# Optimization experiments

Measured on AMD Instinct MI355X. Metric: run time of the kernel, lower is better.

Reference implementation:

```python
import jax, jax.numpy as jnp
import numpy as np

B, C, N = 64, 512, 512  # batch, channels (=in_dim), last dim (=in_dim)
OUT = 512
GROUPS = 32
EPS = 1e-5


def setup_inputs() -> dict:
    key = jax.random.key(0)
    ks = jax.random.split(key, 7)
    s = 1.0 / np.sqrt(C)
    return {
        "x": jax.random.normal(ks[0], (B, C, N), dtype=jnp.float32),
        "q_w": jax.random.normal(ks[1], (OUT, C), dtype=jnp.float32) * s,
        "q_b": jax.random.normal(ks[2], (OUT,), dtype=jnp.float32) * s,
        "k_w": jax.random.normal(ks[3], (OUT, C), dtype=jnp.float32) * s,
        "k_b": jax.random.normal(ks[4], (OUT,), dtype=jnp.float32) * s,
        "v_w": jax.random.normal(ks[5], (OUT, C), dtype=jnp.float32) * s,
        "v_b": jax.random.normal(ks[6], (OUT,), dtype=jnp.float32) * s,
        "gn_w": jnp.ones((C,), dtype=jnp.float32),
        "gn_b": jnp.zeros((C,), dtype=jnp.float32),
    }


def group_norm(x, w, b):
    # x: (B, C, N); 32 groups over channel dim, affine per-channel.
    Bb, Cc, Nn = x.shape
    xg = x.reshape(Bb, GROUPS, -1)
    mean = jnp.mean(xg, axis=-1, keepdims=True)
    var = jnp.var(xg, axis=-1, keepdims=True)
    xn = ((xg - mean) * jax.lax.rsqrt(var + EPS)).reshape(Bb, Cc, Nn)
    return xn * w[None, :, None] + b[None, :, None]


def reference(x, q_w, q_b, k_w, k_b, v_w, v_b, gn_w, gn_b):
    xn = group_norm(x, gn_w, gn_b)  # (B, C, N)
    # nn.Linear applies to the last dim (N == in_dim)
    q = jnp.einsum("bcn,dn->bcd", xn, q_w) + q_b  # (B, C, OUT)
    k = jnp.einsum("bcn,dn->bcd", xn, k_w) + k_b
    v = jnp.einsum("bcn,dn->bcd", xn, v_w) + v_b
    scale = 1.0 / jnp.sqrt(jnp.float32(OUT))
    scores = jnp.einsum("bqd,bkd->bqk", q, k) * scale  # (B, C, C)
    attn = jax.nn.softmax(scores, axis=-1)
    return jnp.einsum("bqk,bkd->bqd", attn, v)  # (B, C, OUT)
```

## Files before the change

kernel.cpp:

```cpp
#include <hip/hip_runtime.h>
#include <cstdint>

#define EPSV 1e-5f
#define SM_SCALE 0.044194173824159216f

typedef unsigned short u16;
typedef __attribute__((ext_vector_type(8))) short short8;
typedef __attribute__((ext_vector_type(4))) float f32x4;
typedef __attribute__((ext_vector_type(4))) unsigned short us4;

__device__ __forceinline__ u16 f2bf(float f) {
  union { float f; uint32_t u; } v; v.f = f;
  return (u16)((v.u + 0x7FFFu + ((v.u >> 16) & 1u)) >> 16);
}

__device__ __forceinline__ void gload_lds16(const void* g, void* l) {
  __builtin_amdgcn_global_load_lds((const __attribute__((address_space(1))) void*)g,
                                   (__attribute__((address_space(3))) void*)l, 16, 0, 0);
}

__device__ __forceinline__ f32x4 mfma16(short8 a, short8 b, f32x4 c) {
  return __builtin_amdgcn_mfma_f32_16x16x32_bf16(a, b, c, 0, 0, 0);
}

#define WAIT_ENTER(N, is_tail)                                      \
  if (is_tail) { asm volatile("s_waitcnt vmcnt(0)" ::: "memory"); } \
  else         { asm volatile("s_waitcnt vmcnt(" #N ")" ::: "memory"); } \
  __builtin_amdgcn_s_barrier();                                     \
  asm volatile("" ::: "memory");

#define WAIT_EXIT()                                                 \
  asm volatile("s_waitcnt lgkmcnt(0)" ::: "memory");                \
  __builtin_amdgcn_s_barrier();                                     \
  asm volatile("" ::: "memory");

__global__ __launch_bounds__(256) void gn_fused_k(const float* __restrict__ x,
                                                  const float* __restrict__ gw,
                                                  const float* __restrict__ gb,
                                                  u16* __restrict__ xn) {
  __shared__ float xs[8192];
  __shared__ float ls[4], lss[4];
  const int bg = blockIdx.x;
  const int g = bg & 31;
  const float* p = x + (size_t)bg * 8192;
  float s = 0.f, ss = 0.f;
#pragma unroll
  for (int i = 0; i < 8; ++i) {
    const int idx = i * 1024 + threadIdx.x * 4;
    float4 v = *reinterpret_cast<const float4*>(p + idx);
    *reinterpret_cast<float4*>(xs + idx) = v;
    s += v.x + v.y + v.z + v.w;
    ss += v.x * v.x + v.y * v.y + v.z * v.z + v.w * v.w;
  }
  for (int off = 32; off; off >>= 1) { s += __shfl_xor(s, off); ss += __shfl_xor(ss, off); }
  const int w = threadIdx.x >> 6;
  if ((threadIdx.x & 63) == 0) { ls[w] = s; lss[w] = ss; }
  __syncthreads();
  s = ls[0] + ls[1] + ls[2] + ls[3];
  ss = lss[0] + lss[1] + lss[2] + lss[3];
  const float inv_n = 1.0f / 8192.f;
  const float mean = s * inv_n;
  const float rstd = rsqrtf(ss * inv_n - mean * mean + EPSV);
#pragma unroll
  for (int j = 0; j < 4; ++j) {
    const int idx = j * 2048 + threadIdx.x * 8;
    const int c = g * 16 + (idx >> 9);
    const float sc = gw[c] * rstd;
    const float sh = gb[c] - mean * sc;
    u16 o[8];
#pragma unroll
    for (int e = 0; e < 8; ++e) o[e] = f2bf(xs[idx + e] * sc + sh);
    *reinterpret_cast<uint4*>(xn + (size_t)bg * 8192 + idx) = *reinterpret_cast<const uint4*>(o);
  }
}

__global__ __launch_bounds__(256) void cast3_k(const float* __restrict__ a,
                                               const float* __restrict__ b2,
                                               const float* __restrict__ c,
                                               u16* __restrict__ oa, u16* __restrict__ ob,
                                               u16* __restrict__ oc) {
  const int which = blockIdx.x >> 7;
  const float* in = which == 0 ? a : (which == 1 ? b2 : c);
  u16* out = which == 0 ? oa : (which == 1 ? ob : oc);
  size_t base = (((size_t)(blockIdx.x & 127)) * 256 + threadIdx.x) * 8;
  float4 v0 = *reinterpret_cast<const float4*>(in + base);
  float4 v1 = *reinterpret_cast<const float4*>(in + base + 4);
  u16 o[8];
  o[0] = f2bf(v0.x); o[1] = f2bf(v0.y); o[2] = f2bf(v0.z); o[3] = f2bf(v0.w);
  o[4] = f2bf(v1.x); o[5] = f2bf(v1.y); o[6] = f2bf(v1.z); o[7] = f2bf(v1.w);
  *reinterpret_cast<uint4*>(out + base) = *reinterpret_cast<const uint4*>(o);
}

__global__ __launch_bounds__(256, 1) void qkv_fused_k(
    const u16* __restrict__ xn, const u16* __restrict__ qw,
    const u16* __restrict__ kw, const u16* __restrict__ vw,
    const float* __restrict__ qb, const float* __restrict__ kb,
    const float* __restrict__ vb,
    u16* __restrict__ Q, u16* __restrict__ K, u16* __restrict__ VT) {
  __shared__ u16 As[2][4096];
  __shared__ u16 Bq[2][4096], Bk[2][4096], Bv[2][4096];
  const int d = blockIdx.x;
  const int t = d >> 3;
  const int b = (d & 7) * 8 + (t >> 4);
  const int tile = t & 15;
  const int tm = (tile >> 2) * 128, tn = (tile & 3) * 128;
  const u16* Ab = xn + (size_t)b * 262144;
  const int tid = threadIdx.x, w = tid >> 6, lane = tid & 63;
  const int wr = (w >> 1) * 64, wc = (w & 1) * 64;
  const int srow = lane >> 2, scol = (lane & 3) * 8;
  f32x4 acc[3][4][4] = {};

#define QKV_STAGE(bb, k0)                                                      \
  {                                                                            \
    _Pragma("unroll")                                                          \
    for (int i = 0; i < 2; ++i) {                                              \
      const int ch = w + i * 4;                                                \
      const size_t ro = (size_t)(tn + ch * 16 + srow) * 512 + (k0) + scol;     \
      gload_lds16(Ab + (size_t)(tm + ch * 16 + srow) * 512 + (k0) + scol,      \
                  &As[bb][ch * 512]);                                          \
      gload_lds16(qw + ro, &Bq[bb][ch * 512]);                                 \
      gload_lds16(kw + ro, &Bk[bb][ch * 512]);                                 \
      gload_lds16(vw + ro, &Bv[bb][ch * 512]);                                 \
    }                                                                          \
  }

  QKV_STAGE(0, 0);
  QKV_STAGE(1, 32);
  for (int ts = 0; ts < 16; ++ts) {
    const int cur = ts & 1;
    WAIT_ENTER(8, ts == 15);
    const int frow = lane & 15, fk = (lane >> 4) * 8;
    short8 af[4];
#pragma unroll
    for (int i = 0; i < 4; ++i)
      af[i] = *reinterpret_cast<const short8*>(&As[cur][(wr + i * 16 + frow) * 32 + fk]);
#pragma unroll
    for (int ni = 0; ni < 4; ++ni) {
      const int bo = (wc + ni * 16 + frow) * 32 + fk;
      short8 bq = *reinterpret_cast<const short8*>(&Bq[cur][bo]);
      short8 bk2 = *reinterpret_cast<const short8*>(&Bk[cur][bo]);
      short8 bv2 = *reinterpret_cast<const short8*>(&Bv[cur][bo]);
#pragma unroll
      for (int mi = 0; mi < 4; ++mi) {
        acc[0][mi][ni] = mfma16(af[mi], bq, acc[0][mi][ni]);
        acc[1][mi][ni] = mfma16(af[mi], bk2, acc[1][mi][ni]);
        acc[2][mi][ni] = mfma16(af[mi], bv2, acc[2][mi][ni]);
      }
    }
    WAIT_EXIT();
    if (ts < 14) QKV_STAGE(cur, (ts + 2) * 32);
  }
#undef QKV_STAGE

  const int col0 = lane & 15, row0 = (lane >> 4) * 4;
#pragma unroll
  for (int mi = 0; mi < 4; ++mi) {
#pragma unroll
    for (int ni = 0; ni < 4; ++ni) {
      const int gc = tn + wc + ni * 16 + col0;
      const int gr0 = tm + wr + mi * 16 + row0;
      const float qbv = qb[gc], kbv = kb[gc], vbv = vb[gc];
      us4 vt;
#pragma unroll
      for (int r = 0; r < 4; ++r) {
        const size_t o = (size_t)b * 262144 + (size_t)(gr0 + r) * 512 + gc;
        Q[o] = f2bf(acc[0][mi][ni][r] + qbv);
        K[o] = f2bf(acc[1][mi][ni][r] + kbv);
        vt[r] = f2bf(acc[2][mi][ni][r] + vbv);
      }
      *reinterpret_cast<us4*>(&VT[(size_t)b * 262144 + (size_t)gc * 512 + gr0]) = vt;
    }
  }
}

__global__ __launch_bounds__(512, 2) void scores_softmax_k(const u16* __restrict__ Q,
                                                           const u16* __restrict__ K,
                                                           u16* __restrict__ P) {
  __shared__ u16 Qs[2][4096];
  __shared__ u16 Ks[2][16384];
  const int d = blockIdx.x;
  const int t = d >> 3;
  const int b = (d & 7) * 8 + (t >> 2);
  const int m0 = (t & 3) * 128;
  const u16* Qb = Q + (size_t)b * 262144 + (size_t)m0 * 512;
  const u16* Kb = K + (size_t)b * 262144;
  u16* Pb = P + (size_t)b * 262144;
  const int tid = threadIdx.x, w = tid >> 6, lane = tid & 63;
  const int srow = lane >> 2, scol = (lane & 3) * 8;
  f32x4 acc[32] = {};

#define SC_STAGE(bb, k0)                                                     \
  {                                                                          \
    _Pragma("unroll")                                                        \
    for (int i = 0; i < 4; ++i) {                                            \
      const int ch = w + i * 8;                                              \
      gload_lds16(Kb + (size_t)(ch * 16 + srow) * 512 + (k0) + scol,         \
                  &Ks[bb][ch * 512]);                                        \
    }                                                                        \
    gload_lds16(Qb + (size_t)(w * 16 + srow) * 512 + (k0) + scol,            \
                &Qs[bb][w * 512]);                                           \
  }

  SC_STAGE(0, 0);
  SC_STAGE(1, 32);
  for (int ts = 0; ts < 16; ++ts) {
    const int cur = ts & 1;
    WAIT_ENTER(5, ts == 15);
    const int frow = lane & 15, fk = (lane >> 4) * 8;
    short8 aq = *reinterpret_cast<const short8*>(&Qs[cur][(w * 16 + frow) * 32 + fk]);
#pragma unroll
    for (int f = 0; f < 32; ++f) {
      short8 bk = *reinterpret_cast<const short8*>(&Ks[cur][(f * 16 + frow) * 32 + fk]);
      acc[f] = mfma16(aq, bk, acc[f]);
    }
    WAIT_EXIT();
    if (ts < 14) SC_STAGE(cur, (ts + 2) * 32);
  }
#undef SC_STAGE

  float pm[4] = {-1e30f, -1e30f, -1e30f, -1e30f};
#pragma unroll
  for (int f = 0; f < 32; ++f)
#pragma unroll
    for (int r = 0; r < 4; ++r) {
      float v = acc[f][r] * SM_SCALE;
      acc[f][r] = v;
      pm[r] = fmaxf(pm[r], v);
    }
#pragma unroll
  for (int off = 1; off < 16; off <<= 1)
#pragma unroll
    for (int r = 0; r < 4; ++r) pm[r] = fmaxf(pm[r], __shfl_xor(pm[r], off));
  float ps[4] = {0.f, 0.f, 0.f, 0.f};
#pragma unroll
  for (int f = 0; f < 32; ++f)
#pragma unroll
    for (int r = 0; r < 4; ++r) {
      float e = __expf(acc[f][r] - pm[r]);
      acc[f][r] = e;
      ps[r] += e;
    }
#pragma unroll
  for (int off = 1; off < 16; off <<= 1)
#pragma unroll
    for (int r = 0; r < 4; ++r) ps[r] += __shfl_xor(ps[r], off);
  float rinv[4];
#pragma unroll
  for (int r = 0; r < 4; ++r) rinv[r] = 1.0f / ps[r];
#pragma unroll
  for (int f = 0; f < 32; ++f) {
    const int gcol = f * 16 + (lane & 15);
#pragma unroll
    for (int r = 0; r < 4; ++r) {
      const int grow = m0 + w * 16 + (lane >> 4) * 4 + r;
      Pb[(size_t)grow * 512 + gcol] = f2bf(acc[f][r] * rinv[r]);
    }
  }
}

__global__ __launch_bounds__(256, 2) void pv_gemm_k(const u16* __restrict__ P,
                                                    const u16* __restrict__ VT,
                                                    float* __restrict__ out) {
  __shared__ u16 As[2][4096];
  __shared__ u16 Bs[2][4096];
  const int d = blockIdx.x;
  const int t = d >> 3;
  const int b = (d & 7) * 8 + (t >> 4);
  const int tile = t & 15;
  const int tm = (tile >> 2) * 128, tn = (tile & 3) * 128;
  const u16* Ab = P + (size_t)b * 262144;
  const u16* Bb = VT + (size_t)b * 262144;
  const int tid = threadIdx.x, w = tid >> 6, lane = tid & 63;
  const int wr = (w >> 1) * 64, wc = (w & 1) * 64;
  const int srow = lane >> 2, scol = (lane & 3) * 8;
  f32x4 acc[4][4] = {};

#define PV_STAGE(bb, k0)                                                     \
  {                                                                          \
    _Pragma("unroll")                                                        \
    for (int i = 0; i < 2; ++i) {                                            \
      const int ch = w + i * 4;                                              \
      gload_lds16(Ab + (size_t)(tm + ch * 16 + srow) * 512 + (k0) + scol,    \
                  &As[bb][ch * 512]);                                        \
      gload_lds16(Bb + (size_t)(tn + ch * 16 + srow) * 512 + (k0) + scol,    \
                  &Bs[bb][ch * 512]);                                        \
    }                                                                        \
  }

  PV_STAGE(0, 0);
  PV_STAGE(1, 32);
  for (int ts = 0; ts < 16; ++ts) {
    const int cur = ts & 1;
    WAIT_ENTER(4, ts == 15);
    const int frow = lane & 15, fk = (lane >> 4) * 8;
    short8 af[4], bf[4];
#pragma unroll
    for (int i = 0; i < 4; ++i) {
      af[i] = *reinterpret_cast<const short8*>(&As[cur][(wr + i * 16 + frow) * 32 + fk]);
      bf[i] = *reinterpret_cast<const short8*>(&Bs[cur][(wc + i * 16 + frow) * 32 + fk]);
    }
#pragma unroll
    for (int mi = 0; mi < 4; ++mi)
#pragma unroll
      for (int ni = 0; ni < 4; ++ni)
        acc[mi][ni] = mfma16(af[mi], bf[ni], acc[mi][ni]);
    WAIT_EXIT();
    if (ts < 14) PV_STAGE(cur, (ts + 2) * 32);
  }
#undef PV_STAGE

  const int col0 = lane & 15, row0 = (lane >> 4) * 4;
#pragma unroll
  for (int mi = 0; mi < 4; ++mi)
#pragma unroll
    for (int ni = 0; ni < 4; ++ni) {
      const int gc = tn + wc + ni * 16 + col0;
#pragma unroll
      for (int r = 0; r < 4; ++r) {
        const int gr = tm + wr + mi * 16 + row0 + r;
        out[(size_t)b * 262144 + (size_t)gr * 512 + gc] = acc[mi][ni][r];
      }
    }
}

extern "C" void kernel_launch(void* const* d_in, const int* in_sizes, int n_in,
                              void* d_out, int out_size, void* d_ws, size_t ws_size,
                              hipStream_t stream) {
  const float* x = (const float*)d_in[0];
  const float* qw = (const float*)d_in[1];
  const float* qb = (const float*)d_in[2];
  const float* kw = (const float*)d_in[3];
  const float* kb = (const float*)d_in[4];
  const float* vw = (const float*)d_in[5];
  const float* vb = (const float*)d_in[6];
  const float* gnw = (const float*)d_in[7];
  const float* gnb = (const float*)d_in[8];

  char* ws = (char*)d_ws;
  u16* qwb = (u16*)(ws);
  u16* kwb = (u16*)(ws + 524288);
  u16* vwb = (u16*)(ws + 2 * 524288);
  u16* xn = (u16*)(ws + 4 * 524288);
  u16* Qb = xn + 16777216;
  u16* Kb = Qb + 16777216;
  u16* VT = Kb + 16777216;
  u16* P = xn;
  float* out = (float*)d_out;

  gn_fused_k<<<dim3(2048), dim3(256), 0, stream>>>(x, gnw, gnb, xn);
  cast3_k<<<dim3(384), dim3(256), 0, stream>>>(qw, kw, vw, qwb, kwb, vwb);
  qkv_fused_k<<<dim3(1024), dim3(256), 0, stream>>>(xn, qwb, kwb, vwb, qb, kb, vb, Qb, Kb, VT);
  scores_softmax_k<<<dim3(256), dim3(512), 0, stream>>>(Qb, Kb, P);
  pv_gemm_k<<<dim3(1024), dim3(256), 0, stream>>>(P, VT, out);
}
```

Baseline: 169.6 us.

## Swizzle LDS layouts, widen QKV blocks, and retile scores kernel with cross-wave softmax

Applies an XOR swizzle to the LDS tile layout in all three GEMM kernels to avoid bank conflicts on fragment reads. The QKV kernel moves to 512 threads with 8 waves, each computing a 64x32 sub-tile, which cuts accumulator registers so two blocks can be resident per CU. The scores kernel is retiled so each wave covers 64 query rows by 128 key columns, which reuses Q fragments across more MFMAs. This requires reducing the softmax row max and sum across four waves through shared memory, adding two block barriers.

```diff
diff --git a/kernel.cpp b/kernel.cpp
--- a/kernel.cpp
+++ b/kernel.cpp
@@ -21,6 +21,10 @@
 
 __device__ __forceinline__ f32x4 mfma16(short8 a, short8 b, f32x4 c) {
   return __builtin_amdgcn_mfma_f32_16x16x32_bf16(a, b, c, 0, 0, 0);
+}
+
+__device__ __forceinline__ const short8* lds_frag(const u16* t, int row, int cc) {
+  return reinterpret_cast<const short8*>(t + (size_t)(((row << 2) + (cc ^ ((row >> 1) & 3))) << 3));
 }
 
 #define WAIT_ENTER(N, is_tail)                                      \
@@ -91,7 +95,7 @@
   *reinterpret_cast<uint4*>(out + base) = *reinterpret_cast<const uint4*>(o);
 }
 
-__global__ __launch_bounds__(256, 1) void qkv_fused_k(
+__global__ __launch_bounds__(512, 2) void qkv_fused_k(
     const u16* __restrict__ xn, const u16* __restrict__ qw,
     const u16* __restrict__ kw, const u16* __restrict__ vw,
     const float* __restrict__ qb, const float* __restrict__ kb,
@@ -105,22 +109,24 @@
   const int tile = t & 15;
   const int tm = (tile >> 2) * 128, tn = (tile & 3) * 128;
   const u16* Ab = xn + (size_t)b * 262144;
-  const int tid = threadIdx.x, w = tid >> 6, lane = tid & 63;
-  const int wr = (w >> 1) * 64, wc = (w & 1) * 64;
-  const int srow = lane >> 2, scol = (lane & 3) * 8;
-  f32x4 acc[3][4][4] = {};
+  const int tid = threadIdx.x, wid = tid >> 6, lane = tid & 63;
+  const int wrow = (wid >> 2) * 64, wcol = (wid & 3) * 32;
+  const int srow = lane >> 2;
+  const int ssw = ((lane & 3) ^ ((lane >> 3) & 3)) * 8;
+  f32x4 acc[3][4][2] = {};
 
 #define QKV_STAGE(bb, k0)                                                      \
   {                                                                            \
     _Pragma("unroll")                                                          \
-    for (int i = 0; i < 2; ++i) {                                              \
-      const int ch = w + i * 4;                                                \
-      const size_t ro = (size_t)(tn + ch * 16 + srow) * 512 + (k0) + scol;     \
-      gload_lds16(Ab + (size_t)(tm + ch * 16 + srow) * 512 + (k0) + scol,      \
-                  &As[bb][ch * 512]);                                          \
-      gload_lds16(qw + ro, &Bq[bb][ch * 512]);                                 \
-      gload_lds16(kw + ro, &Bk[bb][ch * 512]);                                 \
-      gload_lds16(vw + ro, &Bv[bb][ch * 512]);                                 \
+    for (int s2 = 0; s2 < 4; ++s2) {                                           \
+      const int c = wid * 4 + s2;                                              \
+      const int m = c >> 3;                                                    \
+      const int ch = c & 7;                                                    \
+      const size_t gro = (size_t)(ch * 16 + srow) * 512 + (k0) + ssw;          \
+      if (m == 0)      gload_lds16(Ab + (size_t)tm * 512 + gro, &As[bb][ch * 512]); \
+      else if (m == 1) gload_lds16(qw + (size_t)tn * 512 + gro, &Bq[bb][ch * 512]); \
+      else if (m == 2) gload_lds16(kw + (size_t)tn * 512 + gro, &Bk[bb][ch * 512]); \
+      else             gload_lds16(vw + (size_t)tn * 512 + gro, &Bv[bb][ch * 512]); \
     }                                                                          \
   }
 
@@ -128,25 +134,27 @@
   QKV_STAGE(1, 32);
   for (int ts = 0; ts < 16; ++ts) {
     const int cur = ts & 1;
-    WAIT_ENTER(8, ts == 15);
-    const int frow = lane & 15, fk = (lane >> 4) * 8;
-    short8 af[4];
-#pragma unroll
-    for (int i = 0; i < 4; ++i)
-      af[i] = *reinterpret_cast<const short8*>(&As[cur][(wr + i * 16 + frow) * 32 + fk]);
-#pragma unroll
-    for (int ni = 0; ni < 4; ++ni) {
-      const int bo = (wc + ni * 16 + frow) * 32 + fk;
-      short8 bq = *reinterpret_cast<const short8*>(&Bq[cur][bo]);
-      short8 bk2 = *reinterpret_cast<const short8*>(&Bk[cur][bo]);
-      short8 bv2 = *reinterpret_cast<const short8*>(&Bv[cur][bo]);
-#pragma unroll
-      for (int mi = 0; mi < 4; ++mi) {
-        acc[0][mi][ni] = mfma16(af[mi], bq, acc[0][mi][ni]);
-        acc[1][mi][ni] = mfma16(af[mi], bk2, acc[1][mi][ni]);
-        acc[2][mi][ni] = mfma16(af[mi], bv2, acc[2][mi][ni]);
-      }
-    }
+    WAIT_ENTER(4, ts == 15);
+    const int frow = lane & 15, cc = lane >> 4;
+    short8 af[4], b0[2], b1[2], b2[2];
+#pragma unroll
+    for (int i = 0; i < 4; ++i)
+      af[i] = *lds_frag(As[cur], wrow + i * 16 + frow, cc);
+#pragma unroll
+    for (int j = 0; j < 2; ++j) {
+      const int br = wcol + j * 16 + frow;
+      b0[j] = *lds_frag(Bq[cur], br, cc);
+      b1[j] = *lds_frag(Bk[cur], br, cc);
+      b2[j] = *lds_frag(Bv[cur], br, cc);
+    }
+#pragma unroll
+    for (int i = 0; i < 4; ++i)
+#pragma unroll
+      for (int j = 0; j < 2; ++j) {
+        acc[0][i][j] = mfma16(af[i], b0[j], acc[0][i][j]);
+        acc[1][i][j] = mfma16(af[i], b1[j], acc[1][i][j]);
+        acc[2][i][j] = mfma16(af[i], b2[j], acc[2][i][j]);
+      }
     WAIT_EXIT();
     if (ts < 14) QKV_STAGE(cur, (ts + 2) * 32);
   }
@@ -154,19 +162,19 @@
 
   const int col0 = lane & 15, row0 = (lane >> 4) * 4;
 #pragma unroll
-  for (int mi = 0; mi < 4; ++mi) {
-#pragma unroll
-    for (int ni = 0; ni < 4; ++ni) {
-      const int gc = tn + wc + ni * 16 + col0;
-      const int gr0 = tm + wr + mi * 16 + row0;
+  for (int i = 0; i < 4; ++i) {
+#pragma unroll
+    for (int j = 0; j < 2; ++j) {
+      const int gc = tn + wcol + j * 16 + col0;
+      const int gr0 = tm + wrow + i * 16 + row0;
       const float qbv = qb[gc], kbv = kb[gc], vbv = vb[gc];
       us4 vt;
 #pragma unroll
       for (int r = 0; r < 4; ++r) {
         const size_t o = (size_t)b * 262144 + (size_t)(gr0 + r) * 512 + gc;
-        Q[o] = f2bf(acc[0][mi][ni][r] + qbv);
-        K[o] = f2bf(acc[1][mi][ni][r] + kbv);
-        vt[r] = f2bf(acc[2][mi][ni][r] + vbv);
+        Q[o] = f2bf(acc[0][i][j][r] + qbv);
+        K[o] = f2bf(acc[1][i][j][r] + kbv);
+        vt[r] = f2bf(acc[2][i][j][r] + vbv);
       }
       *reinterpret_cast<us4*>(&VT[(size_t)b * 262144 + (size_t)gc * 512 + gr0]) = vt;
     }
@@ -178,6 +186,7 @@
                                                            u16* __restrict__ P) {
   __shared__ u16 Qs[2][4096];
   __shared__ u16 Ks[2][16384];
+  __shared__ float rmax[4][128], rsum[4][128];
   const int d = blockIdx.x;
   const int t = d >> 3;
   const int b = (d & 7) * 8 + (t >> 2);
@@ -185,20 +194,24 @@
   const u16* Qb = Q + (size_t)b * 262144 + (size_t)m0 * 512;
   const u16* Kb = K + (size_t)b * 262144;
   u16* Pb = P + (size_t)b * 262144;
-  const int tid = threadIdx.x, w = tid >> 6, lane = tid & 63;
-  const int srow = lane >> 2, scol = (lane & 3) * 8;
-  f32x4 acc[32] = {};
-
-#define SC_STAGE(bb, k0)                                                     \
-  {                                                                          \
-    _Pragma("unroll")                                                        \
-    for (int i = 0; i < 4; ++i) {                                            \
-      const int ch = w + i * 8;                                              \
-      gload_lds16(Kb + (size_t)(ch * 16 + srow) * 512 + (k0) + scol,         \
-                  &Ks[bb][ch * 512]);                                        \
-    }                                                                        \
-    gload_lds16(Qb + (size_t)(w * 16 + srow) * 512 + (k0) + scol,            \
-                &Qs[bb][w * 512]);                                           \
+  const int tid = threadIdx.x, wid = tid >> 6, lane = tid & 63;
+  const int qh = wid >> 2, kq = wid & 3;
+  const int srow = lane >> 2;
+  const int ssw = ((lane & 3) ^ ((lane >> 3) & 3)) * 8;
+  f32x4 acc[4][8] = {};
+
+#define SC_STAGE(bb, k0)                                                       \
+  {                                                                            \
+    _Pragma("unroll")                                                          \
+    for (int s2 = 0; s2 < 5; ++s2) {                                           \
+      const int c = wid * 5 + s2;                                              \
+      if (c < 8)                                                               \
+        gload_lds16(Qb + (size_t)(c * 16 + srow) * 512 + (k0) + ssw,           \
+                    &Qs[bb][c * 512]);                                         \
+      else                                                                     \
+        gload_lds16(Kb + (size_t)((c - 8) * 16 + srow) * 512 + (k0) + ssw,     \
+                    &Ks[bb][(c - 8) * 512]);                                   \
+    }                                                                          \
   }
 
   SC_STAGE(0, 0);
@@ -206,56 +219,106 @@
   for (int ts = 0; ts < 16; ++ts) {
     const int cur = ts & 1;
     WAIT_ENTER(5, ts == 15);
-    const int frow = lane & 15, fk = (lane >> 4) * 8;
-    short8 aq = *reinterpret_cast<const short8*>(&Qs[cur][(w * 16 + frow) * 32 + fk]);
-#pragma unroll
-    for (int f = 0; f < 32; ++f) {
-      short8 bk = *reinterpret_cast<const short8*>(&Ks[cur][(f * 16 + frow) * 32 + fk]);
-      acc[f] = mfma16(aq, bk, acc[f]);
+    const int frow = lane & 15, cc = lane >> 4;
+    short8 aq[4];
+#pragma unroll
+    for (int i = 0; i < 4; ++i)
+      aq[i] = *lds_frag(Qs[cur], qh * 64 + i * 16 + frow, cc);
+#pragma unroll
+    for (int j = 0; j < 8; ++j) {
+      short8 bk = *lds_frag(Ks[cur], kq * 128 + j * 16 + frow, cc);
+#pragma unroll
+      for (int i = 0; i < 4; ++i)
+        acc[i][j] = mfma16(aq[i], bk, acc[i][j]);
     }
     WAIT_EXIT();
     if (ts < 14) SC_STAGE(cur, (ts + 2) * 32);
   }
 #undef SC_STAGE
 
-  float pm[4] = {-1e30f, -1e30f, -1e30f, -1e30f};
-#pragma unroll
-  for (int f = 0; f < 32; ++f)
+  float pm[4][4];
+#pragma unroll
+  for (int i = 0; i < 4; ++i)
+#pragma unroll
+    for (int r = 0; r < 4; ++r) pm[i][r] = -1e30f;
+#pragma unroll
+  for (int i = 0; i < 4; ++i)
+#pragma unroll
+    for (int j = 0; j < 8; ++j)
+#pragma unroll
+      for (int r = 0; r < 4; ++r) {
+        float v = acc[i][j][r] * SM_SCALE;
+        acc[i][j][r] = v;
+        pm[i][r] = fmaxf(pm[i][r], v);
+      }
+#pragma unroll
+  for (int off = 1; off < 16; off <<= 1)
+#pragma unroll
+    for (int i = 0; i < 4; ++i)
+#pragma unroll
+      for (int r = 0; r < 4; ++r) pm[i][r] = fmaxf(pm[i][r], __shfl_xor(pm[i][r], off));
+  if ((lane & 15) == 0) {
+#pragma unroll
+    for (int i = 0; i < 4; ++i)
+#pragma unroll
+      for (int r = 0; r < 4; ++r)
+        rmax[kq][qh * 64 + i * 16 + (lane >> 4) * 4 + r] = pm[i][r];
+  }
+  __syncthreads();
+#pragma unroll
+  for (int i = 0; i < 4; ++i)
 #pragma unroll
     for (int r = 0; r < 4; ++r) {
-      float v = acc[f][r] * SM_SCALE;
-      acc[f][r] = v;
-      pm[r] = fmaxf(pm[r], v);
-    }
+      const int row = qh * 64 + i * 16 + (lane >> 4) * 4 + r;
+      pm[i][r] = fmaxf(fmaxf(rmax[0][row], rmax[1][row]), fmaxf(rmax[2][row], rmax[3][row]));
+    }
+  float ps[4][4];
+#pragma unroll
+  for (int i = 0; i < 4; ++i)
+#pragma unroll
+    for (int r = 0; r < 4; ++r) ps[i][r] = 0.f;
+#pragma unroll
+  for (int i = 0; i < 4; ++i)
+#pragma unroll
+    for (int j = 0; j < 8; ++j)
+#pragma unroll
+      for (int r = 0; r < 4; ++r) {
+        float e = __expf(acc[i][j][r] - pm[i][r]);
+        acc[i][j][r] = e;
+        ps[i][r] += e;
+      }
 #pragma unroll
   for (int off = 1; off < 16; off <<= 1)
 #pragma unroll
-    for (int r = 0; r < 4; ++r) pm[r] = fmaxf(pm[r], __shfl_xor(pm[r], off));
-  float ps[4] = {0.f, 0.f, 0.f, 0.f};
-#pragma unroll
-  for (int f = 0; f < 32; ++f)
+    for (int i = 0; i < 4; ++i)
+#pragma unroll
+      for (int r = 0; r < 4; ++r) ps[i][r] += __shfl_xor(ps[i][r], off);
+  if ((lane & 15) == 0) {
+#pragma unroll
+    for (int i = 0; i < 4; ++i)
+#pragma unroll
+      for (int r = 0; r < 4; ++r)
+        rsum[kq][qh * 64 + i * 16 + (lane >> 4) * 4 + r] = ps[i][r];
+  }
+  __syncthreads();
+#pragma unroll
+  for (int i = 0; i < 4; ++i)
 #pragma unroll
     for (int r = 0; r < 4; ++r) {
-      float e = __expf(acc[f][r] - pm[r]);
-      acc[f][r] = e;
-      ps[r] += e;
-    }
-#pragma unroll
-  for (int off = 1; off < 16; off <<= 1)
-#pragma unroll
-    for (int r = 0; r < 4; ++r) ps[r] += __shfl_xor(ps[r], off);
-  float rinv[4];
-#pragma unroll
-  for (int r = 0; r < 4; ++r) rinv[r] = 1.0f / ps[r];
-#pragma unroll
-  for (int f = 0; f < 32; ++f) {
-    const int gcol = f * 16 + (lane & 15);
-#pragma unroll
-    for (int r = 0; r < 4; ++r) {
-      const int grow = m0 + w * 16 + (lane >> 4) * 4 + r;
-      Pb[(size_t)grow * 512 + gcol] = f2bf(acc[f][r] * rinv[r]);
-    }
-  }
+      const int row = qh * 64 + i * 16 + (lane >> 4) * 4 + r;
+      ps[i][r] = 1.0f / (rsum[0][row] + rsum[1][row] + rsum[2][row] + rsum[3][row]);
+    }
+#pragma unroll
+  for (int i = 0; i < 4; ++i)
+#pragma unroll
+    for (int j = 0; j < 8; ++j) {
+      const int gcol = kq * 128 + j * 16 + (lane & 15);
+#pragma unroll
+      for (int r = 0; r < 4; ++r) {
+        const int grow = m0 + qh * 64 + i * 16 + (lane >> 4) * 4 + r;
+        Pb[(size_t)grow * 512 + gcol] = f2bf(acc[i][j][r] * ps[i][r]);
+      }
+    }
 }
 
 __global__ __launch_bounds__(256, 2) void pv_gemm_k(const u16* __restrict__ P,
@@ -272,19 +335,22 @@
   const u16* Bb = VT + (size_t)b * 262144;
   const int tid = threadIdx.x, w = tid >> 6, lane = tid & 63;
   const int wr = (w >> 1) * 64, wc = (w & 1) * 64;
-  const int srow = lane >> 2, scol = (lane & 3) * 8;
+  const int srow = lane >> 2;
+  const int ssw = ((lane & 3) ^ ((lane >> 3) & 3)) * 8;
   f32x4 acc[4][4] = {};
 
-#define PV_STAGE(bb, k0)                                                     \
-  {                                                                          \
-    _Pragma("unroll")                                                        \
-    for (int i = 0; i < 2; ++i) {                                            \
-      const int ch = w + i * 4;                                              \
-      gload_lds16(Ab + (size_t)(tm + ch * 16 + srow) * 512 + (k0) + scol,    \
-                  &As[bb][ch * 512]);                                        \
-      gload_lds16(Bb + (size_t)(tn + ch * 16 + srow) * 512 + (k0) + scol,    \
-                  &Bs[bb][ch * 512]);                                        \
-    }                                                                        \
+#define PV_STAGE(bb, k0)                                                       \
+  {                                                                            \
+    _Pragma("unroll")                                                          \
+    for (int s2 = 0; s2 < 4; ++s2) {                                           \
+      const int c = w * 4 + s2;                                                \
+      if (c < 8)                                                               \
+        gload_lds16(Ab + (size_t)(tm + c * 16 + srow) * 512 + (k0) + ssw,      \
+                    &As[bb][c * 512]);                                         \
+      else                                                                     \
+        gload_lds16(Bb + (size_t)(tn + (c - 8) * 16 + srow) * 512 + (k0) + ssw,\
+                    &Bs[bb][(c - 8) * 512]);                                   \
+    }                                                                          \
   }
 
   PV_STAGE(0, 0);
@@ -292,12 +358,12 @@
   for (int ts = 0; ts < 16; ++ts) {
     const int cur = ts & 1;
     WAIT_ENTER(4, ts == 15);
-    const int frow = lane & 15, fk = (lane >> 4) * 8;
+    const int frow = lane & 15, cc = lane >> 4;
     short8 af[4], bf[4];
 #pragma unroll
     for (int i = 0; i < 4; ++i) {
-      af[i] = *reinterpret_cast<const short8*>(&As[cur][(wr + i * 16 + frow) * 32 + fk]);
-      bf[i] = *reinterpret_cast<const short8*>(&Bs[cur][(wc + i * 16 + frow) * 32 + fk]);
+      af[i] = *lds_frag(As[cur], wr + i * 16 + frow, cc);
+      bf[i] = *lds_frag(Bs[cur], wc + i * 16 + frow, cc);
     }
 #pragma unroll
     for (int mi = 0; mi < 4; ++mi)
@@ -349,7 +415,7 @@
 
   gn_fused_k<<<dim3(2048), dim3(256), 0, stream>>>(x, gnw, gnb, xn);
   cast3_k<<<dim3(384), dim3(256), 0, stream>>>(qw, kw, vw, qwb, kwb, vwb);
-  qkv_fused_k<<<dim3(1024), dim3(256), 0, stream>>>(xn, qwb, kwb, vwb, qb, kb, vb, Qb, Kb, VT);
+  qkv_fused_k<<<dim3(1024), dim3(512), 0, stream>>>(xn, qwb, kwb, vwb, qb, kb, vb, Qb, Kb, VT);
   scores_softmax_k<<<dim3(256), dim3(512), 0, stream>>>(Qb, Kb, P);
   pv_gemm_k<<<dim3(1024), dim3(256), 0, stream>>>(P, VT, out);
 }
```

Result: slower. 180.6 us (+6.5%).
